# Performance work log

Measured on AMD Instinct MI355X. Metric: run time of the kernel, lower is better.

Reference implementation:

```python
import jax, jax.numpy as jnp
import numpy as np

B, C, H, W = 4, 256, 64, 64
CH = C // 2  # inner channels of the non-local block


def _conv1x1(x, w, b):
    # 1x1 conv == channel-mixing einsum; x: [B,C,H,W], w: [O,C], b: [O]
    return jnp.einsum('oc,bchw->bohw', w, x) + b[None, :, None, None]


def setup_inputs() -> dict:
    key = jax.random.key(0)
    ks = jax.random.split(key, 9)
    s = 0.02  # small init so exp(scores) stays in fp32 range (no max-subtraction in this block)
    return {
        'x':  jax.random.normal(ks[0], (B, C, H, W), dtype=jnp.float32),
        'w1': s * jax.random.normal(ks[1], (CH, C), dtype=jnp.float32),
        'b1': jnp.zeros((CH,), jnp.float32),
        'w2': s * jax.random.normal(ks[2], (CH, C), dtype=jnp.float32),
        'b2': jnp.zeros((CH,), jnp.float32),
        'w3': s * jax.random.normal(ks[3], (CH, C), dtype=jnp.float32),
        'b3': jnp.zeros((CH,), jnp.float32),
        'w4': s * jax.random.normal(ks[4], (C, CH), dtype=jnp.float32),
        'b4': jnp.zeros((C,), jnp.float32),
    }


def reference(x, w1, b1, w2, b2, w3, b3, w4, b4):
    b, c, h, w = x.shape
    n = h * w
    theta = _conv1x1(x, w1, b1).reshape(b, -1, n)  # [B, C/2, N]
    phi   = _conv1x1(x, w2, b2).reshape(b, -1, n)  # [B, C/2, N]
    g     = _conv1x1(x, w3, b3).reshape(b, -1, n)  # [B, C/2, N]
    # full non-local affinity: [B, N, N]
    scores = jnp.einsum('bci,bcj->bij', theta, phi)
    attn = jnp.exp(scores)  # faithful: no max-subtraction in the original
    attn = attn / jnp.sum(attn, axis=1, keepdims=True)  # normalize over dim=1 as written
    y = jnp.einsum('bij,bcj->bci', attn, g)  # [B, C/2, N]
    y = y.reshape(b, -1, h, w)               # [B, C/2, H, W]
    out = _conv1x1(y, w4, b4) + x            # project back to C, residual
    return out
```

## Files before the change

### kernel.cpp

```cpp
#include <hip/hip_runtime.h>

#define DEVI __device__ __forceinline__

typedef __attribute__((ext_vector_type(8))) short bf16x8;
typedef __attribute__((ext_vector_type(4))) short bf16x4;
typedef __attribute__((ext_vector_type(4))) float f32x4;

#define MFMA16 __builtin_amdgcn_mfma_f32_16x16x32_bf16

DEVI short f2bs(float f) {
  union { float f; unsigned u; } v; v.f = f;
  unsigned r = v.u + 0x7fffu + ((v.u >> 16) & 1u);
  return (short)(r >> 16);
}
DEVI float bs2f(short s) {
  union { unsigned u; float f; } v; v.u = ((unsigned)(unsigned short)s) << 16;
  return v.f;
}

DEVI void gload_lds16(const short* g, short* lds) {
  __builtin_amdgcn_global_load_lds(
      (const __attribute__((address_space(1))) unsigned int*)g,
      (__attribute__((address_space(3))) unsigned int*)lds, 16, 0, 0);
}

DEVI void stage_chunk(short* lds, const short* g, int ldg, int tid) {
#pragma unroll
  for (int it = 0; it < 2; ++it) {
    int slot = it * 256 + tid;
    int row  = slot >> 2;
    int ko   = (slot & 3) << 3;
    gload_lds16(g + (size_t)row * ldg + ko, lds + slot * 8);
  }
}

DEVI void stage_chunk64(short* lds, const short* g, int ldg, int tid) {
  int row = tid >> 2, ko = (tid & 3) << 3;
  gload_lds16(g + (size_t)row * ldg + ko, lds + tid * 8);
}

DEVI bf16x8 lds8(const short* p) { return *(const bf16x8*)p; }

DEVI void zero_acc(f32x4 (&a)[4][4]) {
  f32x4 z = {0.f, 0.f, 0.f, 0.f};
#pragma unroll
  for (int i = 0; i < 4; ++i)
#pragma unroll
    for (int j = 0; j < 4; ++j) a[i][j] = z;
}

__global__ __launch_bounds__(256) void k_transpose_cast(const float* __restrict__ x,
                                                        short* __restrict__ xt) {
  __shared__ float t[64][65];
  int b = blockIdx.z;
  int c0 = blockIdx.y * 64;
  int p0 = blockIdx.x * 64;
  int tid = threadIdx.x;
  const float* xb = x + (size_t)b * 256 * 4096;
#pragma unroll
  for (int i = 0; i < 16; ++i) {
    int idx = i * 256 + tid;
    int c = idx >> 6, p = idx & 63;
    t[p][c] = xb[(size_t)(c0 + c) * 4096 + p0 + p];
  }
  __syncthreads();
  short* xtb = xt + ((size_t)b * 4096 + p0) * 256 + c0;
#pragma unroll
  for (int i = 0; i < 16; ++i) {
    int idx = i * 256 + tid;
    int p = idx >> 6, c = idx & 63;
    xtb[(size_t)p * 256 + c] = f2bs(t[p][c]);
  }
}

__global__ __launch_bounds__(256) void k_cast_w(const float* __restrict__ w1,
                                                const float* __restrict__ w2,
                                                const float* __restrict__ w3,
                                                short* __restrict__ w123) {
  int i = blockIdx.x * 256 + threadIdx.x;
  if (i < 384 * 256) {
    int r = i >> 8;
    const float* w = (r < 128) ? w1 : (r < 256 ? w2 : w3);
    w123[i] = f2bs(w[(size_t)(r & 127) * 256 + (i & 255)]);
  }
}

__global__ __launch_bounds__(256) void k_proj(const short* __restrict__ xt,
                                              const short* __restrict__ w123,
                                              const float* __restrict__ b1,
                                              const float* __restrict__ b2,
                                              const float* __restrict__ b3,
                                              short* __restrict__ theta,
                                              short* __restrict__ phi,
                                              short* __restrict__ gbuf) {
  __shared__ short aL[128 * 32];
  __shared__ short bL[128 * 32];
  __shared__ short oL[128 * 136];
  int tid = threadIdx.x;
  int m0 = blockIdx.x * 128;
  int nb = blockIdx.y;
  int b  = blockIdx.z;
  int lane = tid & 63, wid = tid >> 6;
  int col = lane & 15, quad = lane >> 4;
  int wm = (wid >> 1) * 64, wn = (wid & 1) * 64;
  const short* A = xt + ((size_t)b * 4096 + m0) * 256;
  const short* B = w123 + (size_t)nb * 128 * 256;
  f32x4 acc[4][4];
  zero_acc(acc);
  for (int ks = 0; ks < 8; ++ks) {
    __syncthreads();
    stage_chunk(aL, A + ks * 32, 256, tid);
    stage_chunk(bL, B + ks * 32, 256, tid);
    __syncthreads();
    bf16x8 af[4], bf_[4];
#pragma unroll
    for (int mi = 0; mi < 4; ++mi) af[mi] = lds8(&aL[(wm + mi * 16 + col) * 32 + quad * 8]);
#pragma unroll
    for (int ni = 0; ni < 4; ++ni) bf_[ni] = lds8(&bL[(wn + ni * 16 + col) * 32 + quad * 8]);
#pragma unroll
    for (int mi = 0; mi < 4; ++mi)
#pragma unroll
      for (int ni = 0; ni < 4; ++ni)
        acc[mi][ni] = MFMA16(af[mi], bf_[ni], acc[mi][ni], 0, 0, 0);
  }
  const float* bias = (nb == 0) ? b1 : (nb == 1 ? b2 : b3);
  __syncthreads();
#pragma unroll
  for (int mi = 0; mi < 4; ++mi)
#pragma unroll
    for (int ni = 0; ni < 4; ++ni) {
      float bv = bias[wn + ni * 16 + col];
#pragma unroll
      for (int r = 0; r < 4; ++r)
        oL[(wm + mi * 16 + quad * 4 + r) * 136 + wn + ni * 16 + col] = f2bs(acc[mi][ni][r] + bv);
    }
  __syncthreads();
  short* O = ((nb == 0) ? theta : (nb == 1) ? phi : gbuf) + ((size_t)b * 4096 + m0) * 128;
#pragma unroll
  for (int it = 0; it < 8; ++it) {
    int slot = it * 256 + tid;
    int r = slot >> 4, cp = (slot & 15) * 8;
    *(bf16x8*)(O + (size_t)r * 128 + cp) = lds8(&oL[r * 136 + cp]);
  }
}

__global__ __launch_bounds__(256, 2) void k_denom(const short* __restrict__ theta,
                                                  const short* __restrict__ phi,
                                                  float* __restrict__ dpart) {
  __shared__ short phB[2][16384];
  __shared__ float part[1024];
  int tid = threadIdx.x;
  int ib = blockIdx.x, jc = blockIdx.y, b = blockIdx.z;
  int lane = tid & 63, wid = tid >> 6;
  int col = lane & 15, quad = lane >> 4;
  int wm = (wid >> 1) * 64, wn = (wid & 1) * 64;
  const short* T = theta + ((size_t)b * 4096 + ib * 128) * 128;
  const short* P = phi + ((size_t)b * 4096 + (size_t)jc * 1024) * 128;
  short* Lb = &phB[0][0];
#pragma unroll
  for (int ks = 0; ks < 4; ++ks) stage_chunk(Lb + ks * 8192, T + ks * 32, 128, tid);
  __syncthreads();
  bf16x8 ath[4][4];
#pragma unroll
  for (int ks = 0; ks < 4; ++ks)
#pragma unroll
    for (int mi = 0; mi < 4; ++mi)
      ath[ks][mi] = lds8(&Lb[ks * 8192 + (wm + mi * 16 + col) * 32 + quad * 8]);
  __syncthreads();
#pragma unroll
  for (int ks = 0; ks < 4; ++ks) stage_chunk(&phB[0][0] + ks * 4096, P + ks * 32, 128, tid);
  for (int jt = 0; jt < 8; ++jt) {
    int cur = jt & 1;
    __syncthreads();
    if (jt < 7) {
      const short* Pn = P + (size_t)(jt + 1) * 128 * 128;
#pragma unroll
      for (int ks = 0; ks < 4; ++ks) stage_chunk(&phB[cur ^ 1][0] + ks * 4096, Pn + ks * 32, 128, tid);
    }
    f32x4 sacc[4][4];
    zero_acc(sacc);
#pragma unroll
    for (int ks = 0; ks < 4; ++ks) {
      bf16x8 bp[4];
#pragma unroll
      for (int ni = 0; ni < 4; ++ni) bp[ni] = lds8(&phB[cur][ks * 4096 + (wn + ni * 16 + col) * 32 + quad * 8]);
#pragma unroll
      for (int mi = 0; mi < 4; ++mi)
#pragma unroll
        for (int ni = 0; ni < 4; ++ni)
          sacc[mi][ni] = MFMA16(ath[ks][mi], bp[ni], sacc[mi][ni], 0, 0, 0);
    }
#pragma unroll
    for (int ni = 0; ni < 4; ++ni) {
      float s = 0.f;
#pragma unroll
      for (int mi = 0; mi < 4; ++mi)
#pragma unroll
        for (int r = 0; r < 4; ++r) s += __expf(sacc[mi][ni][r]);
      part[((wid >> 1) * 4 + quad) * 128 + wn + ni * 16 + col] = s;
    }
    __syncthreads();
    if (tid < 128) {
      float d = 0.f;
#pragma unroll
      for (int q = 0; q < 8; ++q) d += part[q * 128 + tid];
      dpart[((size_t)(b * 32 + ib)) * 4096 + jc * 1024 + jt * 128 + tid] = d;
    }
  }
}

__global__ __launch_bounds__(256) void k_fold(const short* __restrict__ gbuf,
                                              const float* __restrict__ dpart,
                                              short* __restrict__ gprime) {
  __shared__ float dinv[128];
  __shared__ short t[128 * 136];
  int tid = threadIdx.x;
  int jb = blockIdx.x, b = blockIdx.y;
  int j0 = jb * 128;
  if (tid < 128) {
    float d = 0.f;
    for (int ib = 0; ib < 32; ++ib) d += dpart[((size_t)(b * 32 + ib)) * 4096 + j0 + tid];
    dinv[tid] = 1.0f / d;
  }
  __syncthreads();
  const short* G = gbuf + ((size_t)b * 4096 + j0) * 128;
#pragma unroll
  for (int it = 0; it < 8; ++it) {
    int slot = it * 256 + tid;
    int j = slot >> 4, c8 = (slot & 15) * 8;
    bf16x8 gv = *(const bf16x8*)(G + (size_t)j * 128 + c8);
    float di = dinv[j];
#pragma unroll
    for (int e = 0; e < 8; ++e) t[(c8 + e) * 136 + j] = f2bs(bs2f(gv[e]) * di);
  }
  __syncthreads();
  short* GP = gprime + (size_t)b * 128 * 4096 + j0;
#pragma unroll
  for (int it = 0; it < 8; ++it) {
    int slot = it * 256 + tid;
    int c = slot >> 4, j8 = (slot & 15) * 8;
    *(bf16x8*)(GP + (size_t)c * 4096 + j8) = *(const bf16x8*)&t[c * 136 + j8];
  }
}

__global__ __launch_bounds__(256, 2) void k_attn_pv(const short* __restrict__ theta,
                                                    const short* __restrict__ phi,
                                                    const short* __restrict__ gprime,
                                                    short* __restrict__ ypart) {
  __shared__ short L[40960];
  int tid = threadIdx.x;
  int ib = blockIdx.x, jc = blockIdx.y, b = blockIdx.z;
  int lane = tid & 63, wid = tid >> 6;
  int col = lane & 15, quad = lane >> 4;
  int wm = (wid >> 1) * 64;
  int wnS = (wid & 1) * 32;
  int wnV = (wid & 1) * 64;
  const short* T = theta + ((size_t)b * 4096 + ib * 128) * 128;
  const short* PH = phi + ((size_t)b * 4096 + (size_t)jc * 1024) * 128;
  const short* GP = gprime + (size_t)b * 128 * 4096 + jc * 1024;
  short* pP = L + 32768;
#pragma unroll
  for (int ks = 0; ks < 4; ++ks) stage_chunk(L + ks * 8192, T + ks * 32, 128, tid);
  __syncthreads();
  bf16x8 ath[4][4];
#pragma unroll
  for (int ks = 0; ks < 4; ++ks)
#pragma unroll
    for (int mi = 0; mi < 4; ++mi)
      ath[ks][mi] = lds8(&L[ks * 8192 + (wm + mi * 16 + col) * 32 + quad * 8]);
  __syncthreads();
#pragma unroll
  for (int ks = 0; ks < 4; ++ks) stage_chunk64(L + ks * 2048, PH + ks * 32, 128, tid);
#pragma unroll
  for (int jh = 0; jh < 2; ++jh) stage_chunk(L + 16384 + jh * 4096, GP + jh * 32, 4096, tid);
  f32x4 accy[4][4];
  zero_acc(accy);
  for (int jt = 0; jt < 16; ++jt) {
    int cur = jt & 1;
    short* phc = L + cur * 8192;
    short* phn = L + (cur ^ 1) * 8192;
    short* gpc = L + 16384 + cur * 8192;
    short* gpn = L + 16384 + (cur ^ 1) * 8192;
    __syncthreads();
    if (jt < 15) {
      const short* PHn = PH + (size_t)(jt + 1) * 64 * 128;
#pragma unroll
      for (int ks = 0; ks < 4; ++ks) stage_chunk64(phn + ks * 2048, PHn + ks * 32, 128, tid);
    }
    f32x4 s[4][2];
#pragma unroll
    for (int mi = 0; mi < 4; ++mi)
#pragma unroll
      for (int ni = 0; ni < 2; ++ni) s[mi][ni] = (f32x4){0.f, 0.f, 0.f, 0.f};
#pragma unroll
    for (int ks = 0; ks < 4; ++ks) {
      bf16x8 bp[2];
#pragma unroll
      for (int ni = 0; ni < 2; ++ni) bp[ni] = lds8(&phc[ks * 2048 + (wnS + ni * 16 + col) * 32 + quad * 8]);
#pragma unroll
      for (int mi = 0; mi < 4; ++mi)
#pragma unroll
        for (int ni = 0; ni < 2; ++ni)
          s[mi][ni] = MFMA16(ath[ks][mi], bp[ni], s[mi][ni], 0, 0, 0);
    }
#pragma unroll
    for (int mi = 0; mi < 4; ++mi)
#pragma unroll
      for (int ni = 0; ni < 2; ++ni) {
        int jj = wnS + ni * 16 + col;
        int cj = jj >> 5, jg = (jj >> 3) & 3, jl = jj & 7;
#pragma unroll
        for (int r = 0; r < 4; ++r) {
          int i = wm + mi * 16 + quad * 4 + r;
          pP[cj * 4096 + i * 32 + (((jg ^ (i >> 2)) & 3) << 3) + jl] = f2bs(__expf(s[mi][ni][r]));
        }
      }
    __syncthreads();
    if (jt < 15) {
      const short* GPn = GP + (jt + 1) * 64;
#pragma unroll
      for (int jh = 0; jh < 2; ++jh) stage_chunk(gpn + jh * 4096, GPn + jh * 32, 4096, tid);
    }
#pragma unroll
    for (int ks = 0; ks < 2; ++ks) {
      bf16x8 ap[4], bg[4];
#pragma unroll
      for (int mi = 0; mi < 4; ++mi) {
        int i = wm + mi * 16 + col;
        ap[mi] = lds8(&pP[ks * 4096 + i * 32 + (((quad ^ (i >> 2)) & 3) << 3)]);
      }
#pragma unroll
      for (int ni = 0; ni < 4; ++ni) bg[ni] = lds8(&gpc[ks * 4096 + (wnV + ni * 16 + col) * 32 + quad * 8]);
#pragma unroll
      for (int mi = 0; mi < 4; ++mi)
#pragma unroll
        for (int ni = 0; ni < 4; ++ni)
          accy[mi][ni] = MFMA16(ap[mi], bg[ni], accy[mi][ni], 0, 0, 0);
    }
  }
  short* Yp = ypart + ((size_t)(jc * 4 + b) * 4096 + (size_t)ib * 128) * 128;
#pragma unroll
  for (int half = 0; half < 2; ++half) {
    __syncthreads();
    if ((wid >> 1) == half) {
#pragma unroll
      for (int mi = 0; mi < 4; ++mi)
#pragma unroll
        for (int ni = 0; ni < 4; ++ni)
#pragma unroll
          for (int r = 0; r < 4; ++r)
            pP[(mi * 16 + quad * 4 + r) * 128 + wnV + ni * 16 + col] = f2bs(accy[mi][ni][r]);
    }
    __syncthreads();
#pragma unroll
    for (int it = 0; it < 4; ++it) {
      int slot = it * 256 + tid;
      int r = slot >> 4, c8 = (slot & 15) * 8;
      *(bf16x8*)(Yp + (size_t)(half * 64 + r) * 128 + c8) = lds8(&pP[r * 128 + c8]);
    }
  }
}

__global__ __launch_bounds__(256) void k_out(const short* __restrict__ ypart,
                                             const float* __restrict__ w4,
                                             const float* __restrict__ b4,
                                             const float* __restrict__ x,
                                             float* __restrict__ out) {
  __shared__ short wL[4 * 4096];
  __shared__ short yL[4 * 4096];
  __shared__ float bLs[128];
  int tid = threadIdx.x;
  int ibk = blockIdx.x, ob = blockIdx.y, b = blockIdx.z;
  int o0 = ob * 128, i0 = ibk * 128;
  int lane = tid & 63, wid = tid >> 6;
  int col = lane & 15, quad = lane >> 4;
  int wm = (wid >> 1) * 64, wn = (wid & 1) * 64;
#pragma unroll
  for (int it = 0; it < 16; ++it) {
    int slot = it * 256 + tid;
    int r = slot >> 5, c4 = (slot & 31) * 4;
    int ks = c4 >> 5, cr = c4 & 31;
    f32x4 wv = *(const f32x4*)(w4 + (size_t)(o0 + r) * 128 + c4);
    bf16x4 wp;
#pragma unroll
    for (int e = 0; e < 4; ++e) wp[e] = f2bs(wv[e]);
    *(bf16x4*)&wL[ks * 4096 + r * 32 + cr] = wp;
  }
#pragma unroll
  for (int it = 0; it < 8; ++it) {
    int slot = it * 256 + tid;
    int r = slot >> 4, c8 = (slot & 15) * 8;
    int ks = c8 >> 5, cr = c8 & 31;
    float a8[8];
#pragma unroll
    for (int e = 0; e < 8; ++e) a8[e] = 0.f;
#pragma unroll
    for (int p = 0; p < 4; ++p) {
      bf16x8 v = *(const bf16x8*)(ypart + ((size_t)(p * 4 + b) * 4096 + i0 + r) * 128 + c8);
#pragma unroll
      for (int e = 0; e < 8; ++e) a8[e] += bs2f(v[e]);
    }
    bf16x8 yv;
#pragma unroll
    for (int e = 0; e < 8; ++e) yv[e] = f2bs(a8[e]);
    *(bf16x8*)&yL[ks * 4096 + r * 32 + cr] = yv;
  }
  if (tid < 128) bLs[tid] = b4[o0 + tid];
  __syncthreads();
  f32x4 acc[4][4];
  zero_acc(acc);
#pragma unroll
  for (int ks = 0; ks < 4; ++ks) {
    bf16x8 af[4], bf_[4];
#pragma unroll
    for (int mi = 0; mi < 4; ++mi) af[mi] = lds8(&wL[ks * 4096 + (wm + mi * 16 + col) * 32 + quad * 8]);
#pragma unroll
    for (int ni = 0; ni < 4; ++ni) bf_[ni] = lds8(&yL[ks * 4096 + (wn + ni * 16 + col) * 32 + quad * 8]);
#pragma unroll
    for (int mi = 0; mi < 4; ++mi)
#pragma unroll
      for (int ni = 0; ni < 4; ++ni)
        acc[mi][ni] = MFMA16(af[mi], bf_[ni], acc[mi][ni], 0, 0, 0);
  }
  const float* X = x + ((size_t)b * 256 + o0) * 4096 + i0;
  float* O = out + ((size_t)b * 256 + o0) * 4096 + i0;
#pragma unroll
  for (int mi = 0; mi < 4; ++mi)
#pragma unroll
    for (int ni = 0; ni < 4; ++ni)
#pragma unroll
      for (int r = 0; r < 4; ++r) {
        int o = wm + mi * 16 + quad * 4 + r;
        int i = wn + ni * 16 + col;
        O[(size_t)o * 4096 + i] = acc[mi][ni][r] + X[(size_t)o * 4096 + i] + bLs[o];
      }
}

extern "C" void kernel_launch(void* const* d_in, const int* in_sizes, int n_in,
                              void* d_out, int out_size, void* d_ws, size_t ws_size,
                              hipStream_t stream) {
  const float* x  = (const float*)d_in[0];
  const float* w1 = (const float*)d_in[1];
  const float* b1 = (const float*)d_in[2];
  const float* w2 = (const float*)d_in[3];
  const float* b2 = (const float*)d_in[4];
  const float* w3 = (const float*)d_in[5];
  const float* b3 = (const float*)d_in[6];
  const float* w4 = (const float*)d_in[7];
  const float* b4 = (const float*)d_in[8];
  char* ws = (char*)d_ws;
  short* xt     = (short*)(ws + 0);
  short* w123   = (short*)(ws + 8388608);
  short* theta  = (short*)(ws + 8585216);
  short* phi    = (short*)(ws + 12779520);
  short* gbuf   = (short*)(ws + 16973824);
  short* gprime = (short*)(ws + 21168128);
  float* dpart  = (float*)(ws + 25362432);
  short* ypart  = (short*)(ws + 27459584);
  float* out    = (float*)d_out;
  (void)in_sizes; (void)n_in; (void)out_size; (void)ws_size;

  k_transpose_cast<<<dim3(64, 4, 4), dim3(256), 0, stream>>>(x, xt);
  k_cast_w<<<dim3(384), dim3(256), 0, stream>>>(w1, w2, w3, w123);
  k_proj<<<dim3(32, 3, 4), dim3(256), 0, stream>>>(xt, w123, b1, b2, b3, theta, phi, gbuf);
  k_denom<<<dim3(32, 4, 4), dim3(256), 0, stream>>>(theta, phi, dpart);
  k_fold<<<dim3(32, 4), dim3(256), 0, stream>>>(gbuf, dpart, gprime);
  k_attn_pv<<<dim3(32, 4, 4), dim3(256), 0, stream>>>(theta, phi, gprime, ypart);
  k_out<<<dim3(32, 2, 4), dim3(256), 0, stream>>>(ypart, w4, b4, x, out);
}
```

Measured before the change: 174.0 us.

## XOR-swizzle LDS tiles, transpose score MFMA, and raise priority around MFMA blocks

Applies an XOR swizzle on the k-chunk offset of every LDS-staged bf16 tile, covering the async global_load_lds staging and the manual stores in the output kernel, and reads fragments with the matching swizzle to cut LDS bank conflicts. The attention kernel now computes the score tile transposed (phi as the A operand), so each lane writes four exp values as one packed bf16x4 store into the swizzled P buffer instead of scalar scattered stores. s_setprio brackets are added around MFMA bursts to favour issue of the math-heavy wave. These changes alter several kernels' LDS indexing and must stay consistent between writers and readers.

Measured after the change: 170.8 us. No clear change (-1.9%).

```diff
diff --git a/kernel.cpp b/kernel.cpp
--- a/kernel.cpp
+++ b/kernel.cpp
@@ -24,18 +24,20 @@
       (__attribute__((address_space(3))) unsigned int*)lds, 16, 0, 0);
 }
 
+
 DEVI void stage_chunk(short* lds, const short* g, int ldg, int tid) {
 #pragma unroll
   for (int it = 0; it < 2; ++it) {
     int slot = it * 256 + tid;
     int row  = slot >> 2;
-    int ko   = (slot & 3) << 3;
+    int ko   = ((slot ^ (slot >> 3)) & 3) << 3;
     gload_lds16(g + (size_t)row * ldg + ko, lds + slot * 8);
   }
 }
 
 DEVI void stage_chunk64(short* lds, const short* g, int ldg, int tid) {
-  int row = tid >> 2, ko = (tid & 3) << 3;
+  int row = tid >> 2;
+  int ko  = ((tid ^ (tid >> 3)) & 3) << 3;
   gload_lds16(g + (size_t)row * ldg + ko, lds + tid * 8);
 }
 
@@ -102,6 +104,8 @@
   int b  = blockIdx.z;
   int lane = tid & 63, wid = tid >> 6;
   int col = lane & 15, quad = lane >> 4;
+  int sl = (col >> 1) & 3;
+  int qs = (quad ^ sl) << 3;
   int wm = (wid >> 1) * 64, wn = (wid & 1) * 64;
   const short* A = xt + ((size_t)b * 4096 + m0) * 256;
   const short* B = w123 + (size_t)nb * 128 * 256;
@@ -114,14 +118,16 @@
     __syncthreads();
     bf16x8 af[4], bf_[4];
 #pragma unroll
-    for (int mi = 0; mi < 4; ++mi) af[mi] = lds8(&aL[(wm + mi * 16 + col) * 32 + quad * 8]);
-#pragma unroll
-    for (int ni = 0; ni < 4; ++ni) bf_[ni] = lds8(&bL[(wn + ni * 16 + col) * 32 + quad * 8]);
+    for (int mi = 0; mi < 4; ++mi) af[mi] = lds8(&aL[(wm + mi * 16 + col) * 32 + qs]);
+#pragma unroll
+    for (int ni = 0; ni < 4; ++ni) bf_[ni] = lds8(&bL[(wn + ni * 16 + col) * 32 + qs]);
+    __builtin_amdgcn_s_setprio(1);
 #pragma unroll
     for (int mi = 0; mi < 4; ++mi)
 #pragma unroll
       for (int ni = 0; ni < 4; ++ni)
         acc[mi][ni] = MFMA16(af[mi], bf_[ni], acc[mi][ni], 0, 0, 0);
+    __builtin_amdgcn_s_setprio(0);
   }
   const float* bias = (nb == 0) ? b1 : (nb == 1 ? b2 : b3);
   __syncthreads();
@@ -153,6 +159,8 @@
   int ib = blockIdx.x, jc = blockIdx.y, b = blockIdx.z;
   int lane = tid & 63, wid = tid >> 6;
   int col = lane & 15, quad = lane >> 4;
+  int sl = (col >> 1) & 3;
+  int qs = (quad ^ sl) << 3;
   int wm = (wid >> 1) * 64, wn = (wid & 1) * 64;
   const short* T = theta + ((size_t)b * 4096 + ib * 128) * 128;
   const short* P = phi + ((size_t)b * 4096 + (size_t)jc * 1024) * 128;
@@ -165,7 +173,7 @@
   for (int ks = 0; ks < 4; ++ks)
 #pragma unroll
     for (int mi = 0; mi < 4; ++mi)
-      ath[ks][mi] = lds8(&Lb[ks * 8192 + (wm + mi * 16 + col) * 32 + quad * 8]);
+      ath[ks][mi] = lds8(&Lb[ks * 8192 + (wm + mi * 16 + col) * 32 + qs]);
   __syncthreads();
 #pragma unroll
   for (int ks = 0; ks < 4; ++ks) stage_chunk(&phB[0][0] + ks * 4096, P + ks * 32, 128, tid);
@@ -183,12 +191,14 @@
     for (int ks = 0; ks < 4; ++ks) {
       bf16x8 bp[4];
 #pragma unroll
-      for (int ni = 0; ni < 4; ++ni) bp[ni] = lds8(&phB[cur][ks * 4096 + (wn + ni * 16 + col) * 32 + quad * 8]);
+      for (int ni = 0; ni < 4; ++ni) bp[ni] = lds8(&phB[cur][ks * 4096 + (wn + ni * 16 + col) * 32 + qs]);
+      __builtin_amdgcn_s_setprio(1);
 #pragma unroll
       for (int mi = 0; mi < 4; ++mi)
 #pragma unroll
         for (int ni = 0; ni < 4; ++ni)
           sacc[mi][ni] = MFMA16(ath[ks][mi], bp[ni], sacc[mi][ni], 0, 0, 0);
+      __builtin_amdgcn_s_setprio(0);
     }
 #pragma unroll
     for (int ni = 0; ni < 4; ++ni) {
@@ -252,9 +262,12 @@
   int ib = blockIdx.x, jc = blockIdx.y, b = blockIdx.z;
   int lane = tid & 63, wid = tid >> 6;
   int col = lane & 15, quad = lane >> 4;
+  int sl = (col >> 1) & 3;
+  int qs = (quad ^ sl) << 3;
   int wm = (wid >> 1) * 64;
-  int wnS = (wid & 1) * 32;
-  int wnV = (wid & 1) * 64;
+  int cj = wid & 1;
+  int wnS = cj * 32;
+  int wnV = cj * 64;
   const short* T = theta + ((size_t)b * 4096 + ib * 128) * 128;
   const short* PH = phi + ((size_t)b * 4096 + (size_t)jc * 1024) * 128;
   const short* GP = gprime + (size_t)b * 128 * 4096 + jc * 1024;
@@ -267,7 +280,7 @@
   for (int ks = 0; ks < 4; ++ks)
 #pragma unroll
     for (int mi = 0; mi < 4; ++mi)
-      ath[ks][mi] = lds8(&L[ks * 8192 + (wm + mi * 16 + col) * 32 + quad * 8]);
+      ath[ks][mi] = lds8(&L[ks * 8192 + (wm + mi * 16 + col) * 32 + qs]);
   __syncthreads();
 #pragma unroll
   for (int ks = 0; ks < 4; ++ks) stage_chunk64(L + ks * 2048, PH + ks * 32, 128, tid);
@@ -275,6 +288,7 @@
   for (int jh = 0; jh < 2; ++jh) stage_chunk(L + 16384 + jh * 4096, GP + jh * 32, 4096, tid);
   f32x4 accy[4][4];
   zero_acc(accy);
+  int qh = quad >> 1, ql = (quad & 1) << 2;
   for (int jt = 0; jt < 16; ++jt) {
     int cur = jt & 1;
     short* phc = L + cur * 8192;
@@ -287,33 +301,34 @@
 #pragma unroll
       for (int ks = 0; ks < 4; ++ks) stage_chunk64(phn + ks * 2048, PHn + ks * 32, 128, tid);
     }
-    f32x4 s[4][2];
-#pragma unroll
-    for (int mi = 0; mi < 4; ++mi)
-#pragma unroll
-      for (int ni = 0; ni < 2; ++ni) s[mi][ni] = (f32x4){0.f, 0.f, 0.f, 0.f};
+    f32x4 st[2][4];
+#pragma unroll
+    for (int mj = 0; mj < 2; ++mj)
+#pragma unroll
+      for (int ni = 0; ni < 4; ++ni) st[mj][ni] = (f32x4){0.f, 0.f, 0.f, 0.f};
 #pragma unroll
     for (int ks = 0; ks < 4; ++ks) {
       bf16x8 bp[2];
 #pragma unroll
-      for (int ni = 0; ni < 2; ++ni) bp[ni] = lds8(&phc[ks * 2048 + (wnS + ni * 16 + col) * 32 + quad * 8]);
-#pragma unroll
-      for (int mi = 0; mi < 4; ++mi)
-#pragma unroll
-        for (int ni = 0; ni < 2; ++ni)
-          s[mi][ni] = MFMA16(ath[ks][mi], bp[ni], s[mi][ni], 0, 0, 0);
-    }
-#pragma unroll
-    for (int mi = 0; mi < 4; ++mi)
-#pragma unroll
-      for (int ni = 0; ni < 2; ++ni) {
-        int jj = wnS + ni * 16 + col;
-        int cj = jj >> 5, jg = (jj >> 3) & 3, jl = jj & 7;
-#pragma unroll
-        for (int r = 0; r < 4; ++r) {
-          int i = wm + mi * 16 + quad * 4 + r;
-          pP[cj * 4096 + i * 32 + (((jg ^ (i >> 2)) & 3) << 3) + jl] = f2bs(__expf(s[mi][ni][r]));
-        }
+      for (int mj = 0; mj < 2; ++mj)
+        bp[mj] = lds8(&phc[ks * 2048 + (wnS + mj * 16 + col) * 32 + qs]);
+      __builtin_amdgcn_s_setprio(1);
+#pragma unroll
+      for (int mj = 0; mj < 2; ++mj)
+#pragma unroll
+        for (int ni = 0; ni < 4; ++ni)
+          st[mj][ni] = MFMA16(bp[mj], ath[ks][ni], st[mj][ni], 0, 0, 0);
+      __builtin_amdgcn_s_setprio(0);
+    }
+#pragma unroll
+    for (int mj = 0; mj < 2; ++mj)
+#pragma unroll
+      for (int ni = 0; ni < 4; ++ni) {
+        int i = wm + ni * 16 + col;
+        bf16x4 p4;
+#pragma unroll
+        for (int r = 0; r < 4; ++r) p4[r] = f2bs(__expf(st[mj][ni][r]));
+        *(bf16x4*)&pP[cj * 4096 + i * 32 + ((((mj << 1) + qh) ^ sl) << 3) + ql] = p4;
       }
     __syncthreads();
     if (jt < 15) {
@@ -325,17 +340,18 @@
     for (int ks = 0; ks < 2; ++ks) {
       bf16x8 ap[4], bg[4];
 #pragma unroll
-      for (int mi = 0; mi < 4; ++mi) {
-        int i = wm + mi * 16 + col;
-        ap[mi] = lds8(&pP[ks * 4096 + i * 32 + (((quad ^ (i >> 2)) & 3) << 3)]);
-      }
-#pragma unroll
-      for (int ni = 0; ni < 4; ++ni) bg[ni] = lds8(&gpc[ks * 4096 + (wnV + ni * 16 + col) * 32 + quad * 8]);
+      for (int mi = 0; mi < 4; ++mi)
+        ap[mi] = lds8(&pP[ks * 4096 + (wm + mi * 16 + col) * 32 + qs]);
+#pragma unroll
+      for (int ni = 0; ni < 4; ++ni)
+        bg[ni] = lds8(&gpc[ks * 4096 + (wnV + ni * 16 + col) * 32 + qs]);
+      __builtin_amdgcn_s_setprio(1);
 #pragma unroll
       for (int mi = 0; mi < 4; ++mi)
 #pragma unroll
         for (int ni = 0; ni < 4; ++ni)
           accy[mi][ni] = MFMA16(ap[mi], bg[ni], accy[mi][ni], 0, 0, 0);
+      __builtin_amdgcn_s_setprio(0);
     }
   }
   short* Yp = ypart + ((size_t)(jc * 4 + b) * 4096 + (size_t)ib * 128) * 128;
@@ -374,6 +390,8 @@
   int o0 = ob * 128, i0 = ibk * 128;
   int lane = tid & 63, wid = tid >> 6;
   int col = lane & 15, quad = lane >> 4;
+  int sl = (col >> 1) & 3;
+  int qsw = (quad ^ sl) << 3;
   int wm = (wid >> 1) * 64, wn = (wid & 1) * 64;
 #pragma unroll
   for (int it = 0; it < 16; ++it) {
@@ -384,7 +402,7 @@
     bf16x4 wp;
 #pragma unroll
     for (int e = 0; e < 4; ++e) wp[e] = f2bs(wv[e]);
-    *(bf16x4*)&wL[ks * 4096 + r * 32 + cr] = wp;
+    *(bf16x4*)&wL[ks * 4096 + r * 32 + ((((cr >> 3) ^ ((r >> 1) & 3)) << 3) | (cr & 4))] = wp;
   }
 #pragma unroll
   for (int it = 0; it < 8; ++it) {
@@ -403,7 +421,7 @@
     bf16x8 yv;
 #pragma unroll
     for (int e = 0; e < 8; ++e) yv[e] = f2bs(a8[e]);
-    *(bf16x8*)&yL[ks * 4096 + r * 32 + cr] = yv;
+    *(bf16x8*)&yL[ks * 4096 + r * 32 + (((cr >> 3) ^ ((r >> 1) & 3)) << 3)] = yv;
   }
   if (tid < 128) bLs[tid] = b4[o0 + tid];
   __syncthreads();
@@ -413,9 +431,9 @@
   for (int ks = 0; ks < 4; ++ks) {
     bf16x8 af[4], bf_[4];
 #pragma unroll
-    for (int mi = 0; mi < 4; ++mi) af[mi] = lds8(&wL[ks * 4096 + (wm + mi * 16 + col) * 32 + quad * 8]);
-#pragma unroll
-    for (int ni = 0; ni < 4; ++ni) bf_[ni] = lds8(&yL[ks * 4096 + (wn + ni * 16 + col) * 32 + quad * 8]);
+    for (int mi = 0; mi < 4; ++mi) af[mi] = lds8(&wL[ks * 4096 + (wm + mi * 16 + col) * 32 + qsw]);
+#pragma unroll
+    for (int ni = 0; ni < 4; ++ni) bf_[ni] = lds8(&yL[ks * 4096 + (wn + ni * 16 + col) * 32 + qsw]);
 #pragma unroll
     for (int mi = 0; mi < 4; ++mi)
 #pragma unroll
```
